# Kernel optimization log

Measured on AMD Instinct MI355X. Metric: run time of the kernel, lower is better.

Reference implementation:

```python
import jax, jax.numpy as jnp
import numpy as np

N_NODES = 100000
N_EDGES = 1250000
IN_C, HID_C, OUT_C = 64, 128, 64


def setup_inputs() -> dict:
    key = jax.random.key(0)
    ks = jax.random.split(key, 9)
    x = jax.random.normal(ks[0], (N_NODES, IN_C), dtype=jnp.float32)
    edge_index = jax.random.randint(ks[1], (2, N_EDGES), 0, N_NODES, dtype=jnp.int64)
    s = 0.1
    return {
        "x": x,
        "edge_index": edge_index,
        "W_l0": jax.random.normal(ks[2], (IN_C, HID_C), dtype=jnp.float32) * s,
        "W_r0": jax.random.normal(ks[3], (IN_C, HID_C), dtype=jnp.float32) * s,
        "b_l0": jnp.zeros((HID_C,), dtype=jnp.float32),
        "W_l1": jax.random.normal(ks[4], (HID_C, HID_C), dtype=jnp.float32) * s,
        "W_r1": jax.random.normal(ks[5], (HID_C, HID_C), dtype=jnp.float32) * s,
        "b_l1": jnp.zeros((HID_C,), dtype=jnp.float32),
        "W_out": jax.random.normal(ks[6], (HID_C, OUT_C), dtype=jnp.float32) * s,
        "b_out": jnp.zeros((OUT_C,), dtype=jnp.float32),
    }


def _sage_conv(x, src, dst, W_l, b_l, W_r):
    # mean-aggregate source features onto destination nodes
    agg = jax.ops.segment_sum(x[src], dst, num_segments=N_NODES)  # [N, d]
    deg = jax.ops.segment_sum(jnp.ones((src.shape[0],), x.dtype), dst,
                              num_segments=N_NODES)
    mean = agg / jnp.maximum(deg, 1.0)[:, None]
    # out = lin_l(mean_neighbors) + lin_r(x_self); bias only on lin_l (PyG)
    return mean @ W_l + b_l + x @ W_r


def reference(x, edge_index, W_l0, W_r0, b_l0, W_l1, W_r1, b_l1, W_out, b_out):
    src, dst = edge_index[0], edge_index[1]
    h = jax.nn.relu(_sage_conv(x, src, dst, W_l0, b_l0, W_r0))  # dropout = identity (eval)
    h = jax.nn.relu(_sage_conv(h, src, dst, W_l1, b_l1, W_r1))
    return h @ W_out + b_out
```

## Files before the change

kernel.cpp:

```cpp
#include <hip/hip_runtime.h>

#define N_NODES 100000
#define N_EDGES 1250000
#define IN_C 64
#define HID_C 128
#define OUT_C 64
#define NBUCK 98
#define BCAP 16384
#define PA_EPT 16
#define PA_EPB (256 * PA_EPT)
#define PA_BLOCKS ((N_EDGES + PA_EPB - 1) / PA_EPB)
#define BB_EPT 16

typedef __attribute__((ext_vector_type(8))) short short8;
typedef __attribute__((ext_vector_type(4))) float f32x4;
typedef __attribute__((ext_vector_type(2))) float f32x2;

__device__ __forceinline__ float bflo(unsigned u) { return __uint_as_float(u << 16); }
__device__ __forceinline__ float bfhi(unsigned u) { return __uint_as_float(u & 0xffff0000u); }
__device__ __forceinline__ unsigned short f2bf(float f) {
    unsigned u = __float_as_uint(f);
    return (unsigned short)((u + 0x7fffu + ((u >> 16) & 1u)) >> 16);
}
__device__ __forceinline__ unsigned packbf(float lo, float hi) {
    return ((unsigned)f2bf(hi) << 16) | f2bf(lo);
}
__device__ __forceinline__ f32x2 up2(unsigned u) {
    f32x2 r;
    r[0] = bflo(u);
    r[1] = bfhi(u);
    return r;
}
__device__ __forceinline__ void acc8p(const uint4 u, f32x2* a) {
    a[0] += up2(u.x);
    a[1] += up2(u.y);
    a[2] += up2(u.z);
    a[3] += up2(u.w);
}

#define GLOBAL_AS __attribute__((address_space(1)))
#define LDS_AS __attribute__((address_space(3)))
__device__ __forceinline__ void load_lds16(const void* g, void* l) {
    __builtin_amdgcn_global_load_lds((const GLOBAL_AS void*)g, (LDS_AS void*)l, 16, 0, 0);
}

__global__ __launch_bounds__(256) void bucketize_kernel(const unsigned int* __restrict__ e,
                                                        int* __restrict__ bucketCount,
                                                        unsigned* __restrict__ pairs) {
    __shared__ int cnt[NBUCK];
    __shared__ int base[NBUCK];
    __shared__ int flag_s;
    {
        unsigned v = e[2 * (threadIdx.x & 63) + 1];
        unsigned long long b = __ballot(v != 0u);
        if (threadIdx.x == 0) flag_s = (b == 0ull) ? 1 : 0;
    }
    for (int t = threadIdx.x; t < NBUCK; t += 256) cnt[t] = 0;
    __syncthreads();
    const bool i64 = flag_s != 0;
    const int e0 = blockIdx.x * PA_EPB;
    unsigned s[PA_EPT], d[PA_EPT];
    int rank[PA_EPT];
#pragma unroll
    for (int j = 0; j < PA_EPT; ++j) {
        int i = e0 + j * 256 + threadIdx.x;
        if (i < N_EDGES) {
            s[j] = i64 ? e[2 * i] : e[i];
            d[j] = i64 ? e[2 * (N_EDGES + i)] : e[N_EDGES + i];
            rank[j] = atomicAdd(&cnt[d[j] >> 10], 1);
        }
    }
    __syncthreads();
    for (int t = threadIdx.x; t < NBUCK; t += 256)
        base[t] = atomicAdd(&bucketCount[t], cnt[t]);
    __syncthreads();
#pragma unroll
    for (int j = 0; j < PA_EPT; ++j) {
        int i = e0 + j * 256 + threadIdx.x;
        if (i < N_EDGES) {
            unsigned b = d[j] >> 10;
            pairs[b * BCAP + base[b] + rank[j]] = s[j] | ((d[j] & 1023u) << 17);
        }
    }
}

__global__ __launch_bounds__(1024) void bucket_build_kernel(
    const unsigned* __restrict__ pairs, const int* __restrict__ bucketCount,
    int* __restrict__ csr_off, int* __restrict__ csr_src) {
    __shared__ int deg[1024];
    __shared__ int sc[1024];
    __shared__ int bc[128];
    const int k = blockIdx.x;
    const int tid = threadIdx.x;
    if (tid < 128) bc[tid] = (tid < NBUCK) ? bucketCount[tid] : 0;
    deg[tid] = 0;
    __syncthreads();
    for (int off = 1; off < 128; off <<= 1) {
        int t = (tid >= off && tid < 128) ? bc[tid - off] : 0;
        __syncthreads();
        if (tid < 128) bc[tid] += t;
        __syncthreads();
    }
    const int count = bucketCount[k];
    const int gbase = bc[k] - count;
    if (k == 0 && tid == 0) csr_off[N_NODES] = N_EDGES;

    unsigned sp[BB_EPT];
    int rk[BB_EPT];
#pragma unroll
    for (int j = 0; j < BB_EPT; ++j) {
        int idx = j * 1024 + tid;
        if (idx < count) {
            unsigned u = pairs[(size_t)k * BCAP + idx];
            sp[j] = u;
            rk[j] = atomicAdd(&deg[u >> 17], 1);
        }
    }
    __syncthreads();
    const int own = deg[tid];
    sc[tid] = own;
    __syncthreads();
    for (int off = 1; off < 1024; off <<= 1) {
        int t = (tid >= off) ? sc[tid - off] : 0;
        __syncthreads();
        sc[tid] += t;
        __syncthreads();
    }
    const int excl = sc[tid] - own;
    const int node = k * 1024 + tid;
    if (node < N_NODES) csr_off[node] = gbase + excl;
    __syncthreads();
    deg[tid] = excl;
    __syncthreads();
#pragma unroll
    for (int j = 0; j < BB_EPT; ++j) {
        int idx = j * 1024 + tid;
        if (idx < count) {
            unsigned ld = sp[j] >> 17;
            csr_src[gbase + deg[ld] + rk[j]] = (int)(sp[j] & 0x1FFFFu);
        }
    }
}

#define CVT_X_N (N_NODES * IN_C / 4)
__global__ void cvt_kernel(const float* __restrict__ x, unsigned short* __restrict__ xb,
                           const float* __restrict__ Wl0, const float* __restrict__ Wr0,
                           const float* __restrict__ Wl1, const float* __restrict__ Wr1,
                           const float* __restrict__ Wo, unsigned short* __restrict__ wb) {
    int i = blockIdx.x * blockDim.x + threadIdx.x;
    if (i < CVT_X_N) {
        float4 v = ((const float4*)x)[i];
        unsigned lo = ((unsigned)f2bf(v.y) << 16) | f2bf(v.x);
        unsigned hi = ((unsigned)f2bf(v.w) << 16) | f2bf(v.z);
        ((uint2*)xb)[i] = make_uint2(lo, hi);
        return;
    }
    int j = i - CVT_X_N;
    if (j >= 57344) return;
    float v;
    if (j < 8192) {
        int col = j >> 6, k = j & 63;
        v = Wl0[k * HID_C + col];
    } else if (j < 16384) {
        int jj = j - 8192;
        int col = jj >> 6, k = jj & 63;
        v = Wr0[k * HID_C + col];
    } else if (j < 32768) {
        int jj = j - 16384;
        int col = jj >> 7, k = jj & 127;
        v = Wl1[k * HID_C + col];
    } else if (j < 49152) {
        int jj = j - 32768;
        int col = jj >> 7, k = jj & 127;
        v = Wr1[k * HID_C + col];
    } else {
        int jj = j - 49152;
        int col = jj >> 7, k = jj & 127;
        v = Wo[k * OUT_C + col];
    }
    wb[j] = f2bf(v);
}

__global__ __launch_bounds__(256) void agg0_kernel(
    const unsigned short* __restrict__ xb, const int* __restrict__ off,
    const int* __restrict__ csr_src, unsigned short* __restrict__ mean0b) {
    const int wave = (blockIdx.x * 256 + threadIdx.x) >> 6;
    const int lane = threadIdx.x & 63;
    const int slot = lane >> 3;
    const int c4 = lane & 7;
    const uint4* base = (const uint4*)xb;
#pragma unroll
    for (int n = 0; n < 4; ++n) {
        const int wid = wave * 4 + n;
        if (wid >= N_NODES) return;
        int beg = off[wid], end = off[wid + 1];
        f32x2 a[4] = {{0.f, 0.f}, {0.f, 0.f}, {0.f, 0.f}, {0.f, 0.f}};
        int e = beg + slot;
        for (; e + 8 < end; e += 16) {
            uint4 ua = base[(size_t)csr_src[e] * 8 + c4];
            uint4 ub = base[(size_t)csr_src[e + 8] * 8 + c4];
            acc8p(ua, a);
            acc8p(ub, a);
        }
        if (e < end) acc8p(base[(size_t)csr_src[e] * 8 + c4], a);
#pragma unroll
        for (int j = 0; j < 4; ++j) {
            a[j][0] += __shfl_xor(a[j][0], 8);
            a[j][1] += __shfl_xor(a[j][1], 8);
            a[j][0] += __shfl_xor(a[j][0], 16);
            a[j][1] += __shfl_xor(a[j][1], 16);
            a[j][0] += __shfl_xor(a[j][0], 32);
            a[j][1] += __shfl_xor(a[j][1], 32);
        }
        if (slot == 0) {
            float invd = (end > beg) ? 1.f / (float)(end - beg) : 0.f;
            uint4 o;
            o.x = packbf(a[0][0] * invd, a[0][1] * invd);
            o.y = packbf(a[1][0] * invd, a[1][1] * invd);
            o.z = packbf(a[2][0] * invd, a[2][1] * invd);
            o.w = packbf(a[3][0] * invd, a[3][1] * invd);
            ((uint4*)mean0b)[(size_t)wid * 8 + c4] = o;
        }
    }
}

__global__ __launch_bounds__(256) void agg1_kernel(
    const unsigned short* __restrict__ h0b, const int* __restrict__ off,
    const int* __restrict__ csr_src, unsigned short* __restrict__ mean1b) {
    const int wave = (blockIdx.x * 256 + threadIdx.x) >> 6;
    const int lane = threadIdx.x & 63;
    const int slot = lane >> 4;
    const int c4 = lane & 15;
    const uint4* base = (const uint4*)h0b;
#pragma unroll
    for (int n = 0; n < 4; ++n) {
        const int wid = wave * 4 + n;
        if (wid >= N_NODES) return;
        int beg = off[wid], end = off[wid + 1];
        f32x2 a[4] = {{0.f, 0.f}, {0.f, 0.f}, {0.f, 0.f}, {0.f, 0.f}};
        int e = beg + slot;
        for (; e + 4 < end; e += 8) {
            uint4 ua = base[(size_t)csr_src[e] * 16 + c4];
            uint4 ub = base[(size_t)csr_src[e + 4] * 16 + c4];
            acc8p(ua, a);
            acc8p(ub, a);
        }
        if (e < end) acc8p(base[(size_t)csr_src[e] * 16 + c4], a);
#pragma unroll
        for (int j = 0; j < 4; ++j) {
            a[j][0] += __shfl_xor(a[j][0], 16);
            a[j][1] += __shfl_xor(a[j][1], 16);
            a[j][0] += __shfl_xor(a[j][0], 32);
            a[j][1] += __shfl_xor(a[j][1], 32);
        }
        if (slot == 0) {
            float invd = (end > beg) ? 1.f / (float)(end - beg) : 0.f;
            uint4 o;
            o.x = packbf(a[0][0] * invd, a[0][1] * invd);
            o.y = packbf(a[1][0] * invd, a[1][1] * invd);
            o.z = packbf(a[2][0] * invd, a[2][1] * invd);
            o.w = packbf(a[3][0] * invd, a[3][1] * invd);
            ((uint4*)mean1b)[(size_t)wid * 16 + c4] = o;
        }
    }
}

__global__ __launch_bounds__(512) void gemm0_kernel(
    const unsigned short* __restrict__ mean0b, const unsigned short* __restrict__ xb,
    const unsigned short* __restrict__ WlT, const unsigned short* __restrict__ WrT,
    const float* __restrict__ b0, unsigned short* __restrict__ h0b) {
    __shared__ unsigned short sa[64 * IN_C];
    __shared__ unsigned short sh[64 * IN_C];
    const int wave = threadIdx.x >> 6, lane = threadIdx.x & 63;
    const int r16 = lane & 15, q = lane >> 4;
    const int col = wave * 16 + r16;
    const int node0 = blockIdx.x * 64;

    {
        int t = threadIdx.x;
        int row = t >> 3, seg = t & 7;
        int grow = node0 + row;
        if (grow >= N_NODES) grow = N_NODES - 1;
        size_t soff = (size_t)grow * IN_C + (size_t)((seg ^ (row & 7)) * 8);
        load_lds16(mean0b + soff, sa + t * 8);
        load_lds16(xb + soff, sh + t * 8);
    }

    short8 bl[2], br[2];
#pragma unroll
    for (int s = 0; s < 2; ++s) {
        bl[s] = *(const short8*)(WlT + col * IN_C + s * 32 + q * 8);
        br[s] = *(const short8*)(WrT + col * IN_C + s * 32 + q * 8);
    }
    const float bias = b0[col];

    asm volatile("s_waitcnt vmcnt(0)" ::: "memory");
    __syncthreads();

#pragma unroll
    for (int r = 0; r < 4; ++r) {
        const int lrow = r * 16 + r16;
        const int rsw = lrow & 7;
        short8 am[2], ax[2];
#pragma unroll
        for (int s = 0; s < 2; ++s) {
            int seg = s * 4 + q;
            int off = lrow * IN_C + ((seg ^ rsw) * 8);
            am[s] = *(const short8*)(sa + off);
            ax[s] = *(const short8*)(sh + off);
        }
        f32x4 accA, accB;
        accA[0] = bias; accA[1] = bias; accA[2] = bias; accA[3] = bias;
        accB[0] = 0.f; accB[1] = 0.f; accB[2] = 0.f; accB[3] = 0.f;
#pragma unroll
        for (int s = 0; s < 2; ++s) {
            accA = __builtin_amdgcn_mfma_f32_16x16x32_bf16(am[s], bl[s], accA, 0, 0, 0);
            accB = __builtin_amdgcn_mfma_f32_16x16x32_bf16(ax[s], br[s], accB, 0, 0, 0);
        }
#pragma unroll
        for (int rr = 0; rr < 4; ++rr) {
            int row = node0 + r * 16 + q * 4 + rr;
            if (row < N_NODES)
                h0b[(size_t)row * HID_C + col] = f2bf(fmaxf(accA[rr] + accB[rr], 0.f));
        }
    }
}

__global__ __launch_bounds__(512) void gemm1_kernel(
    const unsigned short* __restrict__ mean1b, const unsigned short* __restrict__ h0b,
    const unsigned short* __restrict__ WlT, const unsigned short* __restrict__ WrT,
    const unsigned short* __restrict__ WoT, const float* __restrict__ b1,
    const float* __restrict__ bo, float* __restrict__ out) {
    __shared__ unsigned short sa[64 * HID_C];
    __shared__ unsigned short sh[64 * HID_C];
    __shared__ unsigned short h1s[64 * HID_C];
    const int wave = threadIdx.x >> 6, lane = threadIdx.x & 63;
    const int r16 = lane & 15, q = lane >> 4;
    const int col = wave * 16 + r16;
    const int node0 = blockIdx.x * 64;

    {
        int t = threadIdx.x;
#pragma unroll
        for (int c = 0; c < 4; ++c) {
            int idx = (c & 1) * 512 + t;
            int row = idx >> 4, seg = idx & 15;
            int grow = node0 + row;
            if (grow >= N_NODES) grow = N_NODES - 1;
            size_t soff = (size_t)grow * HID_C + (size_t)((seg ^ (row & 7)) * 8);
            if (c < 2) load_lds16(mean1b + soff, sa + idx * 8);
            else load_lds16(h0b + soff, sh + idx * 8);
        }
    }

    short8 bw0[4], bw1[4], wo[4];
    const int ct = wave & 3;
    const int wcol = ct * 16 + r16;
#pragma unroll
    for (int s = 0; s < 4; ++s) {
        bw0[s] = *(const short8*)(WlT + col * HID_C + s * 32 + q * 8);
        bw1[s] = *(const short8*)(WrT + col * HID_C + s * 32 + q * 8);
        wo[s] = *(const short8*)(WoT + wcol * HID_C + s * 32 + q * 8);
    }
    const float bias1 = b1[col];
    const float biaso = bo[wcol];

    asm volatile("s_waitcnt vmcnt(0)" ::: "memory");
    __syncthreads();

#pragma unroll
    for (int r = 0; r < 4; ++r) {
        const int lrow = r * 16 + r16;
        const int rsw = lrow & 7;
        short8 am[4], ah[4];
#pragma unroll
        for (int s = 0; s < 4; ++s) {
            int seg = s * 4 + q;
            int off = lrow * HID_C + ((seg ^ rsw) * 8);
            am[s] = *(const short8*)(sa + off);
            ah[s] = *(const short8*)(sh + off);
        }
        f32x4 accA, accB;
        accA[0] = bias1; accA[1] = bias1; accA[2] = bias1; accA[3] = bias1;
        accB[0] = 0.f; accB[1] = 0.f; accB[2] = 0.f; accB[3] = 0.f;
#pragma unroll
        for (int s = 0; s < 4; ++s) {
            accA = __builtin_amdgcn_mfma_f32_16x16x32_bf16(am[s], bw0[s], accA, 0, 0, 0);
            accB = __builtin_amdgcn_mfma_f32_16x16x32_bf16(ah[s], bw1[s], accB, 0, 0, 0);
        }
#pragma unroll
        for (int rr = 0; rr < 4; ++rr) {
            int ar = r * 16 + q * 4 + rr;
            int off = (ar * 256 + col * 2) ^ ((ar & 7) << 4);
            *(unsigned short*)((char*)h1s + off) = f2bf(fmaxf(accA[rr] + accB[rr], 0.f));
        }
    }
    __syncthreads();

#pragma unroll
    for (int t = 0; t < 2; ++t) {
        const int rs = (wave >> 2) + 2 * t;
        f32x4 oa;
        oa[0] = biaso; oa[1] = biaso; oa[2] = biaso; oa[3] = biaso;
#pragma unroll
        for (int s = 0; s < 4; ++s) {
            int ar = rs * 16 + r16;
            int off = (ar * 256 + (s * 32 + q * 8) * 2) ^ ((ar & 7) << 4);
            short8 a = *(const short8*)((const char*)h1s + off);
            oa = __builtin_amdgcn_mfma_f32_16x16x32_bf16(a, wo[s], oa, 0, 0, 0);
        }
#pragma unroll
        for (int rr = 0; rr < 4; ++rr) {
            int row = node0 + rs * 16 + q * 4 + rr;
            if (row < N_NODES) out[(size_t)row * OUT_C + wcol] = oa[rr];
        }
    }
}

extern "C" void kernel_launch(void* const* d_in, const int* in_sizes, int n_in,
                              void* d_out, int out_size, void* d_ws, size_t ws_size,
                              hipStream_t stream) {
    const float* x = (const float*)d_in[0];
    const unsigned int* edge = (const unsigned int*)d_in[1];
    const float* Wl0 = (const float*)d_in[2];
    const float* Wr0 = (const float*)d_in[3];
    const float* bl0 = (const float*)d_in[4];
    const float* Wl1 = (const float*)d_in[5];
    const float* Wr1 = (const float*)d_in[6];
    const float* bl1 = (const float*)d_in[7];
    const float* Wo = (const float*)d_in[8];
    const float* bo = (const float*)d_in[9];
    float* out = (float*)d_out;

    char* w = (char*)d_ws;
    auto alloc = [&](size_t bytes) {
        char* p = w;
        w += (bytes + 255) & ~(size_t)255;
        return p;
    };
    int* bucketCount = (int*)alloc(NBUCK * 4);
    int* csr_off = (int*)alloc((size_t)(N_NODES + 1) * 4);
    int* csr_src = (int*)alloc((size_t)N_EDGES * 4);
    unsigned* pairs = (unsigned*)alloc((size_t)NBUCK * BCAP * 4);
    unsigned short* xb = (unsigned short*)alloc((size_t)N_NODES * IN_C * 2);
    unsigned short* mean0b = (unsigned short*)alloc((size_t)N_NODES * IN_C * 2);
    unsigned short* h0b = (unsigned short*)alloc((size_t)N_NODES * HID_C * 2);
    unsigned short* mean1b = (unsigned short*)alloc((size_t)N_NODES * HID_C * 2);
    unsigned short* wb = (unsigned short*)alloc(57344 * 2);

    const unsigned short* Wl0T = wb;
    const unsigned short* Wr0T = wb + 8192;
    const unsigned short* Wl1T = wb + 16384;
    const unsigned short* Wr1T = wb + 32768;
    const unsigned short* WoT = wb + 49152;

    hipMemsetAsync(bucketCount, 0, NBUCK * 4, stream);
    bucketize_kernel<<<PA_BLOCKS, 256, 0, stream>>>(edge, bucketCount, pairs);
    bucket_build_kernel<<<NBUCK, 1024, 0, stream>>>(pairs, bucketCount, csr_off, csr_src);

    cvt_kernel<<<(CVT_X_N + 57344 + 255) / 256, 256, 0, stream>>>(x, xb, Wl0, Wr0, Wl1, Wr1,
                                                                  Wo, wb);

    const int AGG_BLOCKS = (N_NODES + 15) / 16;
    const int GEMM_BLOCKS = (N_NODES + 63) / 64;

    agg0_kernel<<<AGG_BLOCKS, 256, 0, stream>>>(xb, csr_off, csr_src, mean0b);
    gemm0_kernel<<<GEMM_BLOCKS, 512, 0, stream>>>(mean0b, xb, Wl0T, Wr0T, bl0, h0b);
    agg1_kernel<<<AGG_BLOCKS, 256, 0, stream>>>(h0b, csr_off, csr_src, mean1b);
    gemm1_kernel<<<GEMM_BLOCKS, 512, 0, stream>>>(mean1b, h0b, Wl1T, Wr1T, WoT, bl1, bo, out);
}
```

Measured before the change: 181.9 us.

## Fuse mean aggregation into GEMM kernels and merge conversion into bucketize

Moves the neighbor mean aggregation for each layer inside the corresponding GEMM kernel, so each block gathers its 64 destination rows straight into LDS. This removes the mean0b and mean1b global round-trips and two kernel launches. It also folds the bf16 conversion of x and the weights into extra blocks of the bucketize kernel, dropping another launch. The trade-off is fewer, larger blocks doing the irregular gathers: 8 nodes per wave with a fixed 512-thread block and higher LDS use, which may reduce occupancy and latency hiding for the gathers.

```diff
diff --git a/kernel.cpp b/kernel.cpp
--- a/kernel.cpp
+++ b/kernel.cpp
@@ -11,6 +11,8 @@
 #define PA_EPB (256 * PA_EPT)
 #define PA_BLOCKS ((N_EDGES + PA_EPB - 1) / PA_EPB)
 #define BB_EPT 16
+#define CVT_X_N (N_NODES * IN_C / 4)
+#define CVT_BLOCKS ((CVT_X_N + 57344 + 255) / 256)
 
 typedef __attribute__((ext_vector_type(8))) short short8;
 typedef __attribute__((ext_vector_type(4))) float f32x4;
@@ -44,12 +46,51 @@
     __builtin_amdgcn_global_load_lds((const GLOBAL_AS void*)g, (LDS_AS void*)l, 16, 0, 0);
 }
 
-__global__ __launch_bounds__(256) void bucketize_kernel(const unsigned int* __restrict__ e,
-                                                        int* __restrict__ bucketCount,
-                                                        unsigned* __restrict__ pairs) {
+__global__ __launch_bounds__(256) void bucketize_cvt_kernel(
+    const unsigned int* __restrict__ e, int* __restrict__ bucketCount,
+    unsigned* __restrict__ pairs, const float* __restrict__ x,
+    unsigned short* __restrict__ xb, const float* __restrict__ Wl0,
+    const float* __restrict__ Wr0, const float* __restrict__ Wl1,
+    const float* __restrict__ Wr1, const float* __restrict__ Wo,
+    unsigned short* __restrict__ wb) {
     __shared__ int cnt[NBUCK];
     __shared__ int base[NBUCK];
     __shared__ int flag_s;
+    if (blockIdx.x >= PA_BLOCKS) {
+        int i = (blockIdx.x - PA_BLOCKS) * 256 + threadIdx.x;
+        if (i < CVT_X_N) {
+            float4 v = ((const float4*)x)[i];
+            unsigned lo = ((unsigned)f2bf(v.y) << 16) | f2bf(v.x);
+            unsigned hi = ((unsigned)f2bf(v.w) << 16) | f2bf(v.z);
+            ((uint2*)xb)[i] = make_uint2(lo, hi);
+            return;
+        }
+        int j = i - CVT_X_N;
+        if (j >= 57344) return;
+        float v;
+        if (j < 8192) {
+            int col = j >> 6, k = j & 63;
+            v = Wl0[k * HID_C + col];
+        } else if (j < 16384) {
+            int jj = j - 8192;
+            int col = jj >> 6, k = jj & 63;
+            v = Wr0[k * HID_C + col];
+        } else if (j < 32768) {
+            int jj = j - 16384;
+            int col = jj >> 7, k = jj & 127;
+            v = Wl1[k * HID_C + col];
+        } else if (j < 49152) {
+            int jj = j - 32768;
+            int col = jj >> 7, k = jj & 127;
+            v = Wr1[k * HID_C + col];
+        } else {
+            int jj = j - 49152;
+            int col = jj >> 7, k = jj & 127;
+            v = Wo[k * OUT_C + col];
+        }
+        wb[j] = f2bf(v);
+        return;
+    }
     {
         unsigned v = e[2 * (threadIdx.x & 63) + 1];
         unsigned long long b = __ballot(v != 0u);
@@ -142,133 +183,11 @@
     }
 }
 
-#define CVT_X_N (N_NODES * IN_C / 4)
-__global__ void cvt_kernel(const float* __restrict__ x, unsigned short* __restrict__ xb,
-                           const float* __restrict__ Wl0, const float* __restrict__ Wr0,
-                           const float* __restrict__ Wl1, const float* __restrict__ Wr1,
-                           const float* __restrict__ Wo, unsigned short* __restrict__ wb) {
-    int i = blockIdx.x * blockDim.x + threadIdx.x;
-    if (i < CVT_X_N) {
-        float4 v = ((const float4*)x)[i];
-        unsigned lo = ((unsigned)f2bf(v.y) << 16) | f2bf(v.x);
-        unsigned hi = ((unsigned)f2bf(v.w) << 16) | f2bf(v.z);
-        ((uint2*)xb)[i] = make_uint2(lo, hi);
-        return;
-    }
-    int j = i - CVT_X_N;
-    if (j >= 57344) return;
-    float v;
-    if (j < 8192) {
-        int col = j >> 6, k = j & 63;
-        v = Wl0[k * HID_C + col];
-    } else if (j < 16384) {
-        int jj = j - 8192;
-        int col = jj >> 6, k = jj & 63;
-        v = Wr0[k * HID_C + col];
-    } else if (j < 32768) {
-        int jj = j - 16384;
-        int col = jj >> 7, k = jj & 127;
-        v = Wl1[k * HID_C + col];
-    } else if (j < 49152) {
-        int jj = j - 32768;
-        int col = jj >> 7, k = jj & 127;
-        v = Wr1[k * HID_C + col];
-    } else {
-        int jj = j - 49152;
-        int col = jj >> 7, k = jj & 127;
-        v = Wo[k * OUT_C + col];
-    }
-    wb[j] = f2bf(v);
-}
-
-__global__ __launch_bounds__(256) void agg0_kernel(
+__global__ __launch_bounds__(512) void fused0_kernel(
     const unsigned short* __restrict__ xb, const int* __restrict__ off,
-    const int* __restrict__ csr_src, unsigned short* __restrict__ mean0b) {
-    const int wave = (blockIdx.x * 256 + threadIdx.x) >> 6;
-    const int lane = threadIdx.x & 63;
-    const int slot = lane >> 3;
-    const int c4 = lane & 7;
-    const uint4* base = (const uint4*)xb;
-#pragma unroll
-    for (int n = 0; n < 4; ++n) {
-        const int wid = wave * 4 + n;
-        if (wid >= N_NODES) return;
-        int beg = off[wid], end = off[wid + 1];
-        f32x2 a[4] = {{0.f, 0.f}, {0.f, 0.f}, {0.f, 0.f}, {0.f, 0.f}};
-        int e = beg + slot;
-        for (; e + 8 < end; e += 16) {
-            uint4 ua = base[(size_t)csr_src[e] * 8 + c4];
-            uint4 ub = base[(size_t)csr_src[e + 8] * 8 + c4];
-            acc8p(ua, a);
-            acc8p(ub, a);
-        }
-        if (e < end) acc8p(base[(size_t)csr_src[e] * 8 + c4], a);
-#pragma unroll
-        for (int j = 0; j < 4; ++j) {
-            a[j][0] += __shfl_xor(a[j][0], 8);
-            a[j][1] += __shfl_xor(a[j][1], 8);
-            a[j][0] += __shfl_xor(a[j][0], 16);
-            a[j][1] += __shfl_xor(a[j][1], 16);
-            a[j][0] += __shfl_xor(a[j][0], 32);
-            a[j][1] += __shfl_xor(a[j][1], 32);
-        }
-        if (slot == 0) {
-            float invd = (end > beg) ? 1.f / (float)(end - beg) : 0.f;
-            uint4 o;
-            o.x = packbf(a[0][0] * invd, a[0][1] * invd);
-            o.y = packbf(a[1][0] * invd, a[1][1] * invd);
-            o.z = packbf(a[2][0] * invd, a[2][1] * invd);
-            o.w = packbf(a[3][0] * invd, a[3][1] * invd);
-            ((uint4*)mean0b)[(size_t)wid * 8 + c4] = o;
-        }
-    }
-}
-
-__global__ __launch_bounds__(256) void agg1_kernel(
-    const unsigned short* __restrict__ h0b, const int* __restrict__ off,
-    const int* __restrict__ csr_src, unsigned short* __restrict__ mean1b) {
-    const int wave = (blockIdx.x * 256 + threadIdx.x) >> 6;
-    const int lane = threadIdx.x & 63;
-    const int slot = lane >> 4;
-    const int c4 = lane & 15;
-    const uint4* base = (const uint4*)h0b;
-#pragma unroll
-    for (int n = 0; n < 4; ++n) {
-        const int wid = wave * 4 + n;
-        if (wid >= N_NODES) return;
-        int beg = off[wid], end = off[wid + 1];
-        f32x2 a[4] = {{0.f, 0.f}, {0.f, 0.f}, {0.f, 0.f}, {0.f, 0.f}};
-        int e = beg + slot;
-        for (; e + 4 < end; e += 8) {
-            uint4 ua = base[(size_t)csr_src[e] * 16 + c4];
-            uint4 ub = base[(size_t)csr_src[e + 4] * 16 + c4];
-            acc8p(ua, a);
-            acc8p(ub, a);
-        }
-        if (e < end) acc8p(base[(size_t)csr_src[e] * 16 + c4], a);
-#pragma unroll
-        for (int j = 0; j < 4; ++j) {
-            a[j][0] += __shfl_xor(a[j][0], 16);
-            a[j][1] += __shfl_xor(a[j][1], 16);
-            a[j][0] += __shfl_xor(a[j][0], 32);
-            a[j][1] += __shfl_xor(a[j][1], 32);
-        }
-        if (slot == 0) {
-            float invd = (end > beg) ? 1.f / (float)(end - beg) : 0.f;
-            uint4 o;
-            o.x = packbf(a[0][0] * invd, a[0][1] * invd);
-            o.y = packbf(a[1][0] * invd, a[1][1] * invd);
-            o.z = packbf(a[2][0] * invd, a[2][1] * invd);
-            o.w = packbf(a[3][0] * invd, a[3][1] * invd);
-            ((uint4*)mean1b)[(size_t)wid * 16 + c4] = o;
-        }
-    }
-}
-
-__global__ __launch_bounds__(512) void gemm0_kernel(
-    const unsigned short* __restrict__ mean0b, const unsigned short* __restrict__ xb,
-    const unsigned short* __restrict__ WlT, const unsigned short* __restrict__ WrT,
-    const float* __restrict__ b0, unsigned short* __restrict__ h0b) {
+    const int* __restrict__ csr_src, const unsigned short* __restrict__ WlT,
+    const unsigned short* __restrict__ WrT, const float* __restrict__ b0,
+    unsigned short* __restrict__ h0b) {
     __shared__ unsigned short sa[64 * IN_C];
     __shared__ unsigned short sh[64 * IN_C];
     const int wave = threadIdx.x >> 6, lane = threadIdx.x & 63;
@@ -282,7 +201,6 @@
         int grow = node0 + row;
         if (grow >= N_NODES) grow = N_NODES - 1;
         size_t soff = (size_t)grow * IN_C + (size_t)((seg ^ (row & 7)) * 8);
-        load_lds16(mean0b + soff, sa + t * 8);
         load_lds16(xb + soff, sh + t * 8);
     }
 
@@ -293,6 +211,47 @@
         br[s] = *(const short8*)(WrT + col * IN_C + s * 32 + q * 8);
     }
     const float bias = b0[col];
+
+    {
+        const int slot = lane >> 3;
+        const int c4 = lane & 7;
+        const uint4* base = (const uint4*)xb;
+        for (int n = 0; n < 8; ++n) {
+            const int wl = wave * 8 + n;
+            const int wid = node0 + wl;
+            f32x2 a[4] = {{0.f, 0.f}, {0.f, 0.f}, {0.f, 0.f}, {0.f, 0.f}};
+            float invd = 0.f;
+            if (wid < N_NODES) {
+                int beg = off[wid], end = off[wid + 1];
+                int e = beg + slot;
+                for (; e + 8 < end; e += 16) {
+                    uint4 ua = base[(size_t)csr_src[e] * 8 + c4];
+                    uint4 ub = base[(size_t)csr_src[e + 8] * 8 + c4];
+                    acc8p(ua, a);
+                    acc8p(ub, a);
+                }
+                if (e < end) acc8p(base[(size_t)csr_src[e] * 8 + c4], a);
+                invd = (end > beg) ? 1.f / (float)(end - beg) : 0.f;
+            }
+#pragma unroll
+            for (int j = 0; j < 4; ++j) {
+                a[j][0] += __shfl_xor(a[j][0], 8);
+                a[j][1] += __shfl_xor(a[j][1], 8);
+                a[j][0] += __shfl_xor(a[j][0], 16);
+                a[j][1] += __shfl_xor(a[j][1], 16);
+                a[j][0] += __shfl_xor(a[j][0], 32);
+                a[j][1] += __shfl_xor(a[j][1], 32);
+            }
+            if (slot == 0) {
+                uint4 o;
+                o.x = packbf(a[0][0] * invd, a[0][1] * invd);
+                o.y = packbf(a[1][0] * invd, a[1][1] * invd);
+                o.z = packbf(a[2][0] * invd, a[2][1] * invd);
+                o.w = packbf(a[3][0] * invd, a[3][1] * invd);
+                *(uint4*)(&sa[wl * IN_C + ((c4 ^ (wl & 7)) * 8)]) = o;
+            }
+        }
+    }
 
     asm volatile("s_waitcnt vmcnt(0)" ::: "memory");
     __syncthreads();
@@ -305,9 +264,9 @@
 #pragma unroll
         for (int s = 0; s < 2; ++s) {
             int seg = s * 4 + q;
-            int off = lrow * IN_C + ((seg ^ rsw) * 8);
-            am[s] = *(const short8*)(sa + off);
-            ax[s] = *(const short8*)(sh + off);
+            int o = lrow * IN_C + ((seg ^ rsw) * 8);
+            am[s] = *(const short8*)(sa + o);
+            ax[s] = *(const short8*)(sh + o);
         }
         f32x4 accA, accB;
         accA[0] = bias; accA[1] = bias; accA[2] = bias; accA[3] = bias;
@@ -326,11 +285,11 @@
     }
 }
 
-__global__ __launch_bounds__(512) void gemm1_kernel(
-    const unsigned short* __restrict__ mean1b, const unsigned short* __restrict__ h0b,
-    const unsigned short* __restrict__ WlT, const unsigned short* __restrict__ WrT,
-    const unsigned short* __restrict__ WoT, const float* __restrict__ b1,
-    const float* __restrict__ bo, float* __restrict__ out) {
+__global__ __launch_bounds__(512) void fused1_kernel(
+    const unsigned short* __restrict__ h0b, const int* __restrict__ off,
+    const int* __restrict__ csr_src, const unsigned short* __restrict__ WlT,
+    const unsigned short* __restrict__ WrT, const unsigned short* __restrict__ WoT,
+    const float* __restrict__ b1, const float* __restrict__ bo, float* __restrict__ out) {
     __shared__ unsigned short sa[64 * HID_C];
     __shared__ unsigned short sh[64 * HID_C];
     __shared__ unsigned short h1s[64 * HID_C];
@@ -342,14 +301,13 @@
     {
         int t = threadIdx.x;
 #pragma unroll
-        for (int c = 0; c < 4; ++c) {
-            int idx = (c & 1) * 512 + t;
+        for (int c = 0; c < 2; ++c) {
+            int idx = c * 512 + t;
             int row = idx >> 4, seg = idx & 15;
             int grow = node0 + row;
             if (grow >= N_NODES) grow = N_NODES - 1;
             size_t soff = (size_t)grow * HID_C + (size_t)((seg ^ (row & 7)) * 8);
-            if (c < 2) load_lds16(mean1b + soff, sa + idx * 8);
-            else load_lds16(h0b + soff, sh + idx * 8);
+            load_lds16(h0b + soff, sh + idx * 8);
         }
     }
 
@@ -365,6 +323,45 @@
     const float bias1 = b1[col];
     const float biaso = bo[wcol];
 
+    {
+        const int slot = lane >> 4;
+        const int c4 = lane & 15;
+        const uint4* base = (const uint4*)h0b;
+        for (int n = 0; n < 8; ++n) {
+            const int wl = wave * 8 + n;
+            const int wid = node0 + wl;
+            f32x2 a[4] = {{0.f, 0.f}, {0.f, 0.f}, {0.f, 0.f}, {0.f, 0.f}};
+            float invd = 0.f;
+            if (wid < N_NODES) {
+                int beg = off[wid], end = off[wid + 1];
+                int e = beg + slot;
+                for (; e + 4 < end; e += 8) {
+                    uint4 ua = base[(size_t)csr_src[e] * 16 + c4];
+                    uint4 ub = base[(size_t)csr_src[e + 4] * 16 + c4];
+                    acc8p(ua, a);
+                    acc8p(ub, a);
+                }
+                if (e < end) acc8p(base[(size_t)csr_src[e] * 16 + c4], a);
+                invd = (end > beg) ? 1.f / (float)(end - beg) : 0.f;
+            }
+#pragma unroll
+            for (int j = 0; j < 4; ++j) {
+                a[j][0] += __shfl_xor(a[j][0], 16);
+                a[j][1] += __shfl_xor(a[j][1], 16);
+                a[j][0] += __shfl_xor(a[j][0], 32);
+                a[j][1] += __shfl_xor(a[j][1], 32);
+            }
+            if (slot == 0) {
+                uint4 o;
+                o.x = packbf(a[0][0] * invd, a[0][1] * invd);
+                o.y = packbf(a[1][0] * invd, a[1][1] * invd);
+                o.z = packbf(a[2][0] * invd, a[2][1] * invd);
+                o.w = packbf(a[3][0] * invd, a[3][1] * invd);
+                *(uint4*)(&sa[wl * HID_C + ((c4 ^ (wl & 7)) * 8)]) = o;
+            }
+        }
+    }
+
     asm volatile("s_waitcnt vmcnt(0)" ::: "memory");
     __syncthreads();
 
@@ -376,9 +373,9 @@
 #pragma unroll
         for (int s = 0; s < 4; ++s) {
             int seg = s * 4 + q;
-            int off = lrow * HID_C + ((seg ^ rsw) * 8);
-            am[s] = *(const short8*)(sa + off);
-            ah[s] = *(const short8*)(sh + off);
+            int o = lrow * HID_C + ((seg ^ rsw) * 8);
+            am[s] = *(const short8*)(sa + o);
+            ah[s] = *(const short8*)(sh + o);
         }
         f32x4 accA, accB;
         accA[0] = bias1; accA[1] = bias1; accA[2] = bias1; accA[3] = bias1;
@@ -391,8 +388,8 @@
 #pragma unroll
         for (int rr = 0; rr < 4; ++rr) {
             int ar = r * 16 + q * 4 + rr;
-            int off = (ar * 256 + col * 2) ^ ((ar & 7) << 4);
-            *(unsigned short*)((char*)h1s + off) = f2bf(fmaxf(accA[rr] + accB[rr], 0.f));
+            int o = (ar * 256 + col * 2) ^ ((ar & 7) << 4);
+            *(unsigned short*)((char*)h1s + o) = f2bf(fmaxf(accA[rr] + accB[rr], 0.f));
         }
     }
     __syncthreads();
@@ -405,8 +402,8 @@
 #pragma unroll
         for (int s = 0; s < 4; ++s) {
             int ar = rs * 16 + r16;
-            int off = (ar * 256 + (s * 32 + q * 8) * 2) ^ ((ar & 7) << 4);
-            short8 a = *(const short8*)((const char*)h1s + off);
+            int o = (ar * 256 + (s * 32 + q * 8) * 2) ^ ((ar & 7) << 4);
+            short8 a = *(const short8*)((const char*)h1s + o);
             oa = __builtin_amdgcn_mfma_f32_16x16x32_bf16(a, wo[s], oa, 0, 0, 0);
         }
 #pragma unroll
@@ -443,9 +440,7 @@
     int* csr_src = (int*)alloc((size_t)N_EDGES * 4);
     unsigned* pairs = (unsigned*)alloc((size_t)NBUCK * BCAP * 4);
     unsigned short* xb = (unsigned short*)alloc((size_t)N_NODES * IN_C * 2);
-    unsigned short* mean0b = (unsigned short*)alloc((size_t)N_NODES * IN_C * 2);
     unsigned short* h0b = (unsigned short*)alloc((size_t)N_NODES * HID_C * 2);
-    unsigned short* mean1b = (unsigned short*)alloc((size_t)N_NODES * HID_C * 2);
     unsigned short* wb = (unsigned short*)alloc(57344 * 2);
 
     const unsigned short* Wl0T = wb;
@@ -455,17 +450,12 @@
     const unsigned short* WoT = wb + 49152;
 
     hipMemsetAsync(bucketCount, 0, NBUCK * 4, stream);
-    bucketize_kernel<<<PA_BLOCKS, 256, 0, stream>>>(edge, bucketCount, pairs);
+    bucketize_cvt_kernel<<<PA_BLOCKS + CVT_BLOCKS, 256, 0, stream>>>(
+        edge, bucketCount, pairs, x, xb, Wl0, Wr0, Wl1, Wr1, Wo, wb);
     bucket_build_kernel<<<NBUCK, 1024, 0, stream>>>(pairs, bucketCount, csr_off, csr_src);
 
-    cvt_kernel<<<(CVT_X_N + 57344 + 255) / 256, 256, 0, stream>>>(x, xb, Wl0, Wr0, Wl1, Wr1,
-                                                                  Wo, wb);
-
-    const int AGG_BLOCKS = (N_NODES + 15) / 16;
     const int GEMM_BLOCKS = (N_NODES + 63) / 64;
-
-    agg0_kernel<<<AGG_BLOCKS, 256, 0, stream>>>(xb, csr_off, csr_src, mean0b);
-    gemm0_kernel<<<GEMM_BLOCKS, 512, 0, stream>>>(mean0b, xb, Wl0T, Wr0T, bl0, h0b);
-    agg1_kernel<<<AGG_BLOCKS, 256, 0, stream>>>(h0b, csr_off, csr_src, mean1b);
-    gemm1_kernel<<<GEMM_BLOCKS, 512, 0, stream>>>(mean1b, h0b, Wl1T, Wr1T, WoT, bl1, bo, out);
-}
+    fused0_kernel<<<GEMM_BLOCKS, 512, 0, stream>>>(xb, csr_off, csr_src, Wl0T, Wr0T, bl0, h0b);
+    fused1_kernel<<<GEMM_BLOCKS, 512, 0, stream>>>(h0b, csr_off, csr_src, Wl1T, Wr1T, WoT, bl1,
+                                                   bo, out);
+}
```

Result: slower. 207.5 us (+14.0%).
